# Optimization experiments

Hardware: AMD Instinct MI355X
Metric: run time of the kernel (lower is better)

The kernel has to match this reference:

```python
import jax, jax.numpy as jnp
import numpy as np

THRESHOLD_PERCENTILE = 0.8  # init arg
B, H, W, C, N = 4, 256, 256, 128, 32


def _label_components(mask):
    """8-connected components via iterative min-label propagation.
    Background pixels get sentinel label BIG (== scipy label 0)."""
    h, w = mask.shape
    big = h * w
    init = jnp.where(mask, jnp.arange(big, dtype=jnp.int32).reshape(h, w), jnp.int32(big))

    def propagate(lbl):
        p = jnp.pad(lbl, 1, constant_values=big)
        # min over the 3x3 (8-connected incl. self) neighborhood
        nb = jnp.min(jnp.stack([p[di:di + h, dj:dj + w]
                                for di in range(3) for dj in range(3)]), axis=0)
        return jnp.where(mask, nb, jnp.int32(big))

    def cond(state):
        return ~state[1]

    def body(state):
        lbl, _ = state
        new = propagate(lbl)
        return new, jnp.all(new == lbl)

    lbl, _ = jax.lax.while_loop(cond, body, (init, jnp.array(False)))
    return lbl, jnp.int32(big)


def _merged_pairs_one(feat, centers):
    """feat: [H,W,C] float; centers: [N,2] int32. Returns merged-pair count."""
    h, w, c = feat.shape
    gt = feat[centers[:, 0], centers[:, 1]]                    # [N,C]
    flat = feat.reshape(-1, c)                                 # [HW,C]
    # euclidean cdist via norms (torch.cdist p=2)
    d2 = (jnp.sum(flat * flat, axis=1)[:, None]
          + jnp.sum(gt * gt, axis=1)[None, :]
          - 2.0 * flat @ gt.T)                                 # [HW,N]
    dists = jnp.sqrt(jnp.maximum(d2, 0.0))
    contrast = dists.min(axis=1).reshape(h, w)                 # [H,W]
    thr = jnp.percentile(contrast, THRESHOLD_PERCENTILE * 100.0)
    mask = contrast >= thr
    lbl, big = _label_components(mask)
    ids = lbl[centers[:, 0], centers[:, 1]]                    # [N]
    valid = ids != big                                         # scipy label > 0
    eq = (ids[:, None] == ids[None, :]) & valid[:, None]
    n = centers.shape[0]
    triu = jnp.triu(jnp.ones((n, n), dtype=bool), 1)           # i < j pairs
    return jnp.sum(eq & triu)


def setup_inputs() -> dict:
    key = jax.random.key(0)
    k1, k2 = jax.random.split(key)
    features = jax.random.normal(k1, (B, H, W, C), dtype=jnp.float32)
    gt_centers = jax.random.randint(k2, (B, N, 2), 0, H, dtype=jnp.int64)
    return {"features": features, "gt_centers": gt_centers}


def reference(features, gt_centers):
    centers = gt_centers.astype(jnp.int32)
    merged = jax.vmap(_merged_pairs_one)(features, centers)    # [B]
    n = centers.shape[1]
    total_pairs = features.shape[0] * (n * (n - 1) // 2)
    merge_rate = merged.sum().astype(jnp.float32) / jnp.float32(total_pairs)
    return merge_rate
```

## Files before the change

kernel.cpp:

```cpp
#include <hip/hip_runtime.h>
#include <stdint.h>

#define BB 4
#define HH 256
#define WW 256
#define CC 128
#define NN 32
#define NPIX (HH*WW)
#define RANK 52428u
#define TOTAL_PAIRS 1984.0f
#define CAND_MAX 8192u

#define OFF_HIST 0
#define ZERO_BYTES (BB*1024*4)
#define OFF_THR  ZERO_BYTES
#define OFF_P    (OFF_THR + 64)
#define OFF_KEYS (OFF_P + BB*NPIX*4)

typedef __attribute__((ext_vector_type(8))) short short8;
typedef __attribute__((ext_vector_type(4))) float f32x4;

__device__ __forceinline__ void split3(float f, short &hi, short &mid, short &lo) {
    uint32_t u  = __float_as_uint(f);
    uint32_t hb = u & 0xffff0000u;
    hi = (short)(hb >> 16);
    float r1 = f - __uint_as_float(hb);
    uint32_t mb = __float_as_uint(r1) & 0xffff0000u;
    mid = (short)(mb >> 16);
    float r2 = r1 - __uint_as_float(mb);
    lo = (short)(__float_as_uint(r2) >> 16);
}

__device__ __forceinline__ uint32_t qbin_of(uint32_t keybits) {
    float f = __uint_as_float(keybits);
    return (uint32_t)fminf(f * 128.0f, 65535.0f);
}

__global__ __launch_bounds__(256) void k_d2mfma(const float* __restrict__ feat,
        const int* __restrict__ centers, uint32_t* __restrict__ keys,
        uint32_t* __restrict__ hist, int* __restrict__ Pg) {
    __shared__ short gB[12288];
    __shared__ float gpart[32][8];
    __shared__ float gnormL[32];
    __shared__ uint32_t lhist[1024];
    int b = blockIdx.y;
    int tid = threadIdx.x;

    Pg[(b << 16) + blockIdx.x*256 + tid] = 0;

    #pragma unroll
    for (int j = 0; j < 4; j++) lhist[tid + j*256] = 0u;

    {
        int n = tid & 31, j0 = tid >> 5;
        int cy = centers[(b*NN + n)*2 + 0];
        int cx = centers[(b*NN + n)*2 + 1];
        const float* gp = feat + ((size_t)(b << 16) + cy*WW + cx)*CC + j0*16;
        int tt = n >> 4, lane16 = n & 15, q_ = j0 >> 1, kkb = (j0 & 1)*2;
        float ss = 0.f;
        #pragma unroll
        for (int hh = 0; hh < 2; hh++) {
            short8 vhi, vmid, vlo;
            #pragma unroll
            for (int u = 0; u < 8; u++) {
                float f = gp[hh*8 + u];
                ss = fmaf(f, f, ss);
                short a, bm, c; split3(f, a, bm, c);
                vhi[u] = a; vmid[u] = bm; vlo[u] = c;
            }
            int lane = q_*16 + lane16;
            int off = (tt*4 + kkb + hh)*512 + lane*8;
            *(short8*)&gB[off]        = vhi;
            *(short8*)&gB[off + 4096] = vmid;
            *(short8*)&gB[off + 8192] = vlo;
        }
        gpart[n][j0] = ss;
    }
    __syncthreads();
    if (tid < 32) {
        float s = 0.f;
        #pragma unroll
        for (int j = 0; j < 8; j++) s += gpart[tid][j];
        gnormL[tid] = s;
    }
    __syncthreads();

    int wv = tid >> 6, L = tid & 63;
    int m = L & 15, q = L >> 4;
    float gn0 = gnormL[m];
    float gn1 = gnormL[16 + m];

    const float* fpl = feat + ((size_t)(b << 16) + blockIdx.x*256 + m)*CC + q*32;

    float4 pf[8];
    {
        const float* f0 = fpl + (size_t)(wv*4)*16*CC;
        #pragma unroll
        for (int j = 0; j < 8; j++) pf[j] = *(const float4*)(f0 + j*4);
    }

    #pragma unroll
    for (int it = 0; it < 4; it++) {
        int p0 = blockIdx.x*256 + (wv*4 + it)*16;

        float4 nf[8];
        if (it < 3) {
            const float* f1 = fpl + (size_t)(wv*4 + it + 1)*16*CC;
            #pragma unroll
            for (int j = 0; j < 8; j++) nf[j] = *(const float4*)(f1 + j*4);
        }

        f32x4 acc[2] = {{0.f,0.f,0.f,0.f},{0.f,0.f,0.f,0.f}};
        float fn = 0.f;

        #pragma unroll
        for (int kk = 0; kk < 4; kk++) {
            float4 fa = pf[kk*2];
            float4 fb = pf[kk*2 + 1];
            float fs[8] = {fa.x,fa.y,fa.z,fa.w,fb.x,fb.y,fb.z,fb.w};
            short8 ahi, amid, alo;
            #pragma unroll
            for (int j = 0; j < 8; j++) {
                float f = fs[j];
                fn = fmaf(f, f, fn);
                short hh, md, lw; split3(f, hh, md, lw);
                ahi[j] = hh; amid[j] = md; alo[j] = lw;
            }
            #pragma unroll
            for (int t = 0; t < 2; t++) {
                int off = (t*4 + kk)*512 + L*8;
                short8 bhi = *(const short8*)&gB[off];
                short8 bmd = *(const short8*)&gB[off + 4096];
                short8 blo = *(const short8*)&gB[off + 8192];
                acc[t] = __builtin_amdgcn_mfma_f32_16x16x32_bf16(ahi,  bhi, acc[t], 0,0,0);
                acc[t] = __builtin_amdgcn_mfma_f32_16x16x32_bf16(ahi,  bmd, acc[t], 0,0,0);
                acc[t] = __builtin_amdgcn_mfma_f32_16x16x32_bf16(amid, bhi, acc[t], 0,0,0);
                acc[t] = __builtin_amdgcn_mfma_f32_16x16x32_bf16(ahi,  blo, acc[t], 0,0,0);
                acc[t] = __builtin_amdgcn_mfma_f32_16x16x32_bf16(amid, bmd, acc[t], 0,0,0);
                acc[t] = __builtin_amdgcn_mfma_f32_16x16x32_bf16(alo,  bhi, acc[t], 0,0,0);
            }
        }

        fn += __shfl_xor(fn, 16);
        fn += __shfl_xor(fn, 32);

        float vmin[4];
        #pragma unroll
        for (int r = 0; r < 4; r++) {
            float fnr = __shfl(fn, q*4 + r);
            float d0 = fnr + gn0 - 2.f*acc[0][r];
            float d1 = fnr + gn1 - 2.f*acc[1][r];
            float v = fminf(d0, d1);
            v = fminf(v, __shfl_xor(v, 1));
            v = fminf(v, __shfl_xor(v, 2));
            v = fminf(v, __shfl_xor(v, 4));
            v = fminf(v, __shfl_xor(v, 8));
            vmin[r] = v;
        }
        if (m < 4) {
            float v = (m==0) ? vmin[0] : (m==1) ? vmin[1] : (m==2) ? vmin[2] : vmin[3];
            if (!(v > 0.f)) v = 0.f;
            uint32_t kb = __float_as_uint(v);
            keys[(size_t)(b << 16) + p0 + q*4 + m] = kb;
            atomicAdd(&lhist[qbin_of(kb) >> 6], 1u);
        }

        if (it < 3) {
            #pragma unroll
            for (int j = 0; j < 8; j++) pf[j] = nf[j];
        }
    }

    __syncthreads();
    #pragma unroll
    for (int j = 0; j < 4; j++) {
        int bin = tid + j*256;
        uint32_t hv = lhist[bin];
        if (hv) atomicAdd(&hist[(b << 10) + bin], hv);
    }
}

__global__ __launch_bounds__(1024) void k_selthr(const uint32_t* __restrict__ keys,
        const uint32_t* __restrict__ hist, uint32_t* __restrict__ thr_sm) {
    int b = blockIdx.x, t = threadIdx.x;
    __shared__ uint32_t wsum[16];
    __shared__ uint32_t sT1, sR1, sT, sR2, scnt, scnt2;
    __shared__ uint32_t fh[64];
    __shared__ uint32_t cand[CAND_MAX];
    __shared__ uint32_t cand2[2048];

    if (t < 64) fh[t] = 0;
    if (t == 0) { scnt = 0; scnt2 = 0; }

    int lane = t & 63, w = t >> 6;
    uint32_t s = hist[(b << 10) + t];
    uint32_t inc = s;
    #pragma unroll
    for (int off = 1; off < 64; off <<= 1) {
        uint32_t nb = __shfl_up((int)inc, off);
        if (lane >= off) inc += nb;
    }
    if (lane == 63) wsum[w] = inc;
    __syncthreads();
    if (t < 16) {
        uint32_t v = wsum[t];
        #pragma unroll
        for (int off = 1; off < 16; off <<= 1) {
            uint32_t nb = __shfl_up((int)v, off);
            if (t >= off) v += nb;
        }
        wsum[t] = v;
    }
    __syncthreads();
    uint32_t pre = ((w == 0) ? 0u : wsum[w-1]) + inc - s;
    if (pre <= RANK && RANK < pre + s) { sT1 = (uint32_t)t; sR1 = RANK - pre; }
    __syncthreads();
    uint32_t T1 = sT1, r1 = sR1;

    const uint4* kb = (const uint4*)(keys + ((size_t)b << 16));
    for (int i = t; i < NPIX/4; i += 1024) {
        uint4 k = kb[i];
        uint32_t q;
        #define PROC_KEY(X) { q = qbin_of(X); if ((q >> 6) == T1) { \
            atomicAdd(&fh[q & 63u], 1u); \
            uint32_t p = atomicAdd(&scnt, 1u); \
            if (p < CAND_MAX) cand[p] = (X); } }
        PROC_KEY(k.x) PROC_KEY(k.y) PROC_KEY(k.z) PROC_KEY(k.w)
        #undef PROC_KEY
    }
    __syncthreads();

    if (t < 64) {
        uint32_t s2 = fh[t];
        uint32_t inc2 = s2;
        #pragma unroll
        for (int off = 1; off < 64; off <<= 1) {
            uint32_t nb = __shfl_up((int)inc2, off);
            if (t >= off) inc2 += nb;
        }
        uint32_t pre2 = inc2 - s2;
        if (pre2 <= r1 && r1 < pre2 + s2) { sT = (T1 << 6) | (uint32_t)t; sR2 = r1 - pre2; }
    }
    __syncthreads();
    uint32_t T = sT, r2 = sR2;
    uint32_t K = scnt; if (K > CAND_MAX) K = CAND_MAX;

    for (uint32_t i = t; i < K; i += 1024) {
        uint32_t v = cand[i];
        if (qbin_of(v) == T) { uint32_t p = atomicAdd(&scnt2, 1u); if (p < 2048u) cand2[p] = v; }
    }
    __syncthreads();
    uint32_t K2 = scnt2; if (K2 > 2048u) K2 = 2048u;

    for (uint32_t i = t; i < K2; i += 1024) {
        uint32_t v = cand2[i];
        uint32_t less = 0, eq = 0;
        for (uint32_t j = 0; j < K2; j++) { uint32_t x = cand2[j]; less += (x < v); eq += (x == v); }
        if (less <= r2 && r2 < less + eq) thr_sm[b] = v;
    }
}

__device__ __forceinline__ int uf_find(int* P, int x) {
    while (true) {
        int v = P[x];
        if (v == 0) return x;
        int p = v - 1;
        int gv = P[p];
        if (gv == 0) return p;
        P[x] = gv;
        x = gv - 1;
    }
}
__device__ __forceinline__ void uf_unite(int* P, int a, int b) {
    while (true) {
        a = uf_find(P, a);
        b = uf_find(P, b);
        if (a == b) return;
        if (a > b) { int t = a; a = b; b = t; }
        int old = atomicCAS(&P[b], 0, a + 1);
        if (old == 0) return;
        b = old - 1;
    }
}

__global__ __launch_bounds__(256) void k_ccl(const uint32_t* __restrict__ keys,
        const uint32_t* __restrict__ thr_sm, int* __restrict__ Pg) {
    int bid = blockIdx.x;
    int b = bid >> 8, rr = bid & 255;
    int x = threadIdx.x;
    __shared__ int up_rs[256];
    __shared__ int swtmp[4];

    uint32_t thrv = thr_sm[b];
    int* P = Pg + (b << 16);
    int p = (rr << 8) + x;
    bool msk = keys[((size_t)b << 16) + p] >= thrv;
    int lane = x & 63, w = x >> 6;

    int v = msk ? -1 : x;
    #pragma unroll
    for (int off = 1; off < 64; off <<= 1) {
        int nb = __shfl_up(v, off);
        if (lane >= off) v = max(v, nb);
    }
    if (lane == 63) swtmp[w] = v;
    __syncthreads();
    int acc = v;
    for (int i = 0; i < w; i++) acc = max(acc, swtmp[i]);
    int rs = (rr << 8) + acc + 1;
    __syncthreads();

    if (rr > 0) {
        bool msku = keys[((size_t)b << 16) + p - WW] >= thrv;
        int vu = msku ? -1 : x;
        #pragma unroll
        for (int off = 1; off < 64; off <<= 1) {
            int nb = __shfl_up(vu, off);
            if (lane >= off) vu = max(vu, nb);
        }
        if (lane == 63) swtmp[w] = vu;
        __syncthreads();
        int accu = vu;
        for (int i = 0; i < w; i++) accu = max(accu, swtmp[i]);
        up_rs[x] = msku ? (((rr - 1) << 8) + accu + 1) : -1;
    }

    if (msk && rs != p) P[p] = rs + 1;
    __syncthreads();

    if (rr > 0 && msk) {
        bool ul = (x > 0)   && up_rs[x-1] >= 0;
        bool uu =              up_rs[x]   >= 0;
        bool ur = (x < 255) && up_rs[x+1] >= 0;
        if (ul)        uf_unite(P, rs, up_rs[x-1]);
        if (uu && !ul) uf_unite(P, rs, up_rs[x]);
        if (ur && !uu) uf_unite(P, rs, up_rs[x+1]);
    }
}

__global__ void k_pairs_fin(const int* __restrict__ centers,
        const uint32_t* __restrict__ keys, const uint32_t* __restrict__ thr_sm,
        const int* __restrict__ Pg, float* __restrict__ out) {
    __shared__ int ids[BB*NN];
    __shared__ int total;
    int t = threadIdx.x;
    if (t == 0) total = 0;
    __syncthreads();
    if (t < BB*NN) {
        int bb = t >> 5;
        int cy = centers[t*2 + 0];
        int cx = centers[t*2 + 1];
        int pp = cy*WW + cx;
        const int* Pb = Pg + (bb << 16);
        int id = -1;
        if (keys[((size_t)bb << 16) + pp] >= thr_sm[bb]) {
            int xx = pp;
            while (true) { int vv = Pb[xx]; if (vv == 0) break; xx = vv - 1; }
            id = xx;
        }
        ids[t] = id;
    }
    __syncthreads();
    int cnt = 0;
    if (t < BB*NN) {
        int bb = t >> 5, n = t & 31;
        int id = ids[t];
        if (id != -1) for (int j = n + 1; j < NN; j++) cnt += (ids[bb*NN + j] == id);
    }
    if (cnt) atomicAdd(&total, cnt);
    __syncthreads();
    if (t == 0) out[0] = (float)total / TOTAL_PAIRS;
}

extern "C" void kernel_launch(void* const* d_in, const int* in_sizes, int n_in,
                              void* d_out, int out_size, void* d_ws, size_t ws_size,
                              hipStream_t stream) {
    const float* feat  = (const float*)d_in[0];
    const int* centers = (const int*)d_in[1];
    float* out         = (float*)d_out;
    char* ws           = (char*)d_ws;

    uint32_t* hist = (uint32_t*)(ws + OFF_HIST);
    uint32_t* thr  = (uint32_t*)(ws + OFF_THR);
    int*      Pg   = (int*)(ws + OFF_P);
    uint32_t* keys = (uint32_t*)(ws + OFF_KEYS);

    hipMemsetAsync(ws, 0, ZERO_BYTES, stream);

    dim3 gridPix(NPIX/256, BB);
    k_d2mfma    <<<gridPix, 256, 0, stream>>>(feat, centers, keys, hist, Pg);
    k_selthr    <<<BB, 1024, 0, stream>>>(keys, hist, thr);
    k_ccl       <<<HH*BB, 256, 0, stream>>>(keys, thr, Pg);
    k_pairs_fin <<<1, 256, 0, stream>>>(centers, keys, thr, Pg, out);
}
```

Before: 224.6 us.

## Fuse threshold selection, CCL and pair counting into one per-image kernel

Merges the threshold-select, connected-component labeling and pair-count kernels into a single kernel with one 1024-thread block per image, and uses a global done-counter so the last block writes the result. This removes two kernel launches and the global threshold round-trip. The labeling loses the row-scan prepass and the 1024-block parallelism: only 4 blocks now do union-find over 65536 pixels each, neighbor by neighbor, so labeling may take much longer.

```diff
diff --git a/kernel.cpp b/kernel.cpp
--- a/kernel.cpp
+++ b/kernel.cpp
@@ -12,9 +12,9 @@
 #define CAND_MAX 8192u
 
 #define OFF_HIST 0
-#define ZERO_BYTES (BB*1024*4)
-#define OFF_THR  ZERO_BYTES
-#define OFF_P    (OFF_THR + 64)
+#define OFF_SYNC (BB*1024*4)
+#define ZERO_BYTES (OFF_SYNC + 256)
+#define OFF_P    ZERO_BYTES
 #define OFF_KEYS (OFF_P + BB*NPIX*4)
 
 typedef __attribute__((ext_vector_type(8))) short short8;
@@ -180,17 +180,44 @@
     }
 }
 
-__global__ __launch_bounds__(1024) void k_selthr(const uint32_t* __restrict__ keys,
-        const uint32_t* __restrict__ hist, uint32_t* __restrict__ thr_sm) {
+__device__ __forceinline__ int uf_find(int* P, int x) {
+    while (true) {
+        int v = P[x];
+        if (v == 0) return x;
+        int p = v - 1;
+        int gv = P[p];
+        if (gv == 0) return p;
+        P[x] = gv;
+        x = gv - 1;
+    }
+}
+__device__ __forceinline__ void uf_unite(int* P, int a, int b) {
+    while (true) {
+        a = uf_find(P, a);
+        b = uf_find(P, b);
+        if (a == b) return;
+        if (a > b) { int t = a; a = b; b = t; }
+        int old = atomicCAS(&P[b], 0, a + 1);
+        if (old == 0) return;
+        b = old - 1;
+    }
+}
+
+__global__ __launch_bounds__(1024) void k_tail(const uint32_t* __restrict__ keys,
+        const uint32_t* __restrict__ hist, const int* __restrict__ centers,
+        int* __restrict__ Pg, uint32_t* __restrict__ done, int* __restrict__ gcount,
+        float* __restrict__ out) {
     int b = blockIdx.x, t = threadIdx.x;
     __shared__ uint32_t wsum[16];
-    __shared__ uint32_t sT1, sR1, sT, sR2, scnt, scnt2;
+    __shared__ uint32_t sT1, sR1, sT, sR2, scnt, scnt2, sThr;
     __shared__ uint32_t fh[64];
     __shared__ uint32_t cand[CAND_MAX];
     __shared__ uint32_t cand2[2048];
+    __shared__ int ids[NN];
+    __shared__ int blkcnt;
 
     if (t < 64) fh[t] = 0;
-    if (t == 0) { scnt = 0; scnt2 = 0; }
+    if (t == 0) { scnt = 0; scnt2 = 0; blkcnt = 0; }
 
     int lane = t & 63, w = t >> 6;
     uint32_t s = hist[(b << 10) + t];
@@ -256,120 +283,56 @@
         uint32_t v = cand2[i];
         uint32_t less = 0, eq = 0;
         for (uint32_t j = 0; j < K2; j++) { uint32_t x = cand2[j]; less += (x < v); eq += (x == v); }
-        if (less <= r2 && r2 < less + eq) thr_sm[b] = v;
-    }
-}
-
-__device__ __forceinline__ int uf_find(int* P, int x) {
-    while (true) {
-        int v = P[x];
-        if (v == 0) return x;
-        int p = v - 1;
-        int gv = P[p];
-        if (gv == 0) return p;
-        P[x] = gv;
-        x = gv - 1;
-    }
-}
-__device__ __forceinline__ void uf_unite(int* P, int a, int b) {
-    while (true) {
-        a = uf_find(P, a);
-        b = uf_find(P, b);
-        if (a == b) return;
-        if (a > b) { int t = a; a = b; b = t; }
-        int old = atomicCAS(&P[b], 0, a + 1);
-        if (old == 0) return;
-        b = old - 1;
-    }
-}
-
-__global__ __launch_bounds__(256) void k_ccl(const uint32_t* __restrict__ keys,
-        const uint32_t* __restrict__ thr_sm, int* __restrict__ Pg) {
-    int bid = blockIdx.x;
-    int b = bid >> 8, rr = bid & 255;
-    int x = threadIdx.x;
-    __shared__ int up_rs[256];
-    __shared__ int swtmp[4];
-
-    uint32_t thrv = thr_sm[b];
+        if (less <= r2 && r2 < less + eq) sThr = v;
+    }
+    __syncthreads();
+    uint32_t thrv = sThr;
+
+    const uint32_t* kf = keys + ((size_t)b << 16);
     int* P = Pg + (b << 16);
-    int p = (rr << 8) + x;
-    bool msk = keys[((size_t)b << 16) + p] >= thrv;
-    int lane = x & 63, w = x >> 6;
-
-    int v = msk ? -1 : x;
-    #pragma unroll
-    for (int off = 1; off < 64; off <<= 1) {
-        int nb = __shfl_up(v, off);
-        if (lane >= off) v = max(v, nb);
-    }
-    if (lane == 63) swtmp[w] = v;
-    __syncthreads();
-    int acc = v;
-    for (int i = 0; i < w; i++) acc = max(acc, swtmp[i]);
-    int rs = (rr << 8) + acc + 1;
-    __syncthreads();
-
-    if (rr > 0) {
-        bool msku = keys[((size_t)b << 16) + p - WW] >= thrv;
-        int vu = msku ? -1 : x;
-        #pragma unroll
-        for (int off = 1; off < 64; off <<= 1) {
-            int nb = __shfl_up(vu, off);
-            if (lane >= off) vu = max(vu, nb);
-        }
-        if (lane == 63) swtmp[w] = vu;
-        __syncthreads();
-        int accu = vu;
-        for (int i = 0; i < w; i++) accu = max(accu, swtmp[i]);
-        up_rs[x] = msku ? (((rr - 1) << 8) + accu + 1) : -1;
-    }
-
-    if (msk && rs != p) P[p] = rs + 1;
-    __syncthreads();
-
-    if (rr > 0 && msk) {
-        bool ul = (x > 0)   && up_rs[x-1] >= 0;
-        bool uu =              up_rs[x]   >= 0;
-        bool ur = (x < 255) && up_rs[x+1] >= 0;
-        if (ul)        uf_unite(P, rs, up_rs[x-1]);
-        if (uu && !ul) uf_unite(P, rs, up_rs[x]);
-        if (ur && !uu) uf_unite(P, rs, up_rs[x+1]);
-    }
-}
-
-__global__ void k_pairs_fin(const int* __restrict__ centers,
-        const uint32_t* __restrict__ keys, const uint32_t* __restrict__ thr_sm,
-        const int* __restrict__ Pg, float* __restrict__ out) {
-    __shared__ int ids[BB*NN];
-    __shared__ int total;
-    int t = threadIdx.x;
-    if (t == 0) total = 0;
-    __syncthreads();
-    if (t < BB*NN) {
-        int bb = t >> 5;
-        int cy = centers[t*2 + 0];
-        int cx = centers[t*2 + 1];
+    for (int i = t; i < NPIX; i += 1024) {
+        if (kf[i] < thrv) continue;
+        int x = i & 255, y = i >> 8;
+        if (x > 0 && kf[i-1] >= thrv) uf_unite(P, i, i-1);
+        if (y > 0) {
+            if (kf[i-WW] >= thrv)              uf_unite(P, i, i-WW);
+            if (x > 0   && kf[i-WW-1] >= thrv) uf_unite(P, i, i-WW-1);
+            if (x < 255 && kf[i-WW+1] >= thrv) uf_unite(P, i, i-WW+1);
+        }
+    }
+    __syncthreads();
+
+    if (t < NN) {
+        int cy = centers[(b*NN + t)*2 + 0];
+        int cx = centers[(b*NN + t)*2 + 1];
         int pp = cy*WW + cx;
-        const int* Pb = Pg + (bb << 16);
         int id = -1;
-        if (keys[((size_t)bb << 16) + pp] >= thr_sm[bb]) {
+        if (kf[pp] >= thrv) {
             int xx = pp;
-            while (true) { int vv = Pb[xx]; if (vv == 0) break; xx = vv - 1; }
+            while (true) { int vv = P[xx]; if (vv == 0) break; xx = vv - 1; }
             id = xx;
         }
         ids[t] = id;
     }
     __syncthreads();
     int cnt = 0;
-    if (t < BB*NN) {
-        int bb = t >> 5, n = t & 31;
+    if (t < NN) {
         int id = ids[t];
-        if (id != -1) for (int j = n + 1; j < NN; j++) cnt += (ids[bb*NN + j] == id);
-    }
-    if (cnt) atomicAdd(&total, cnt);
-    __syncthreads();
-    if (t == 0) out[0] = (float)total / TOTAL_PAIRS;
+        if (id != -1) for (int j = t + 1; j < NN; j++) cnt += (ids[j] == id);
+    }
+    if (cnt) atomicAdd(&blkcnt, cnt);
+    __syncthreads();
+
+    if (t == 0) {
+        atomicAdd(gcount, blkcnt);
+        __threadfence();
+        uint32_t d = atomicAdd(done, 1u);
+        if (d == 3u) {
+            __threadfence();
+            int total = atomicAdd(gcount, 0);
+            out[0] = (float)total / TOTAL_PAIRS;
+        }
+    }
 }
 
 extern "C" void kernel_launch(void* const* d_in, const int* in_sizes, int n_in,
@@ -380,16 +343,15 @@
     float* out         = (float*)d_out;
     char* ws           = (char*)d_ws;
 
-    uint32_t* hist = (uint32_t*)(ws + OFF_HIST);
-    uint32_t* thr  = (uint32_t*)(ws + OFF_THR);
-    int*      Pg   = (int*)(ws + OFF_P);
-    uint32_t* keys = (uint32_t*)(ws + OFF_KEYS);
+    uint32_t* hist   = (uint32_t*)(ws + OFF_HIST);
+    uint32_t* done   = (uint32_t*)(ws + OFF_SYNC);
+    int*      gcount = (int*)(ws + OFF_SYNC + 4);
+    int*      Pg     = (int*)(ws + OFF_P);
+    uint32_t* keys   = (uint32_t*)(ws + OFF_KEYS);
 
     hipMemsetAsync(ws, 0, ZERO_BYTES, stream);
 
     dim3 gridPix(NPIX/256, BB);
-    k_d2mfma    <<<gridPix, 256, 0, stream>>>(feat, centers, keys, hist, Pg);
-    k_selthr    <<<BB, 1024, 0, stream>>>(keys, hist, thr);
-    k_ccl       <<<HH*BB, 256, 0, stream>>>(keys, thr, Pg);
-    k_pairs_fin <<<1, 256, 0, stream>>>(centers, keys, thr, Pg, out);
-}
+    k_d2mfma <<<gridPix, 256, 0, stream>>>(feat, centers, keys, hist, Pg);
+    k_tail   <<<BB, 1024, 0, stream>>>(keys, hist, centers, Pg, done, gcount, out);
+}
```

Result: slower. 678.7 us (+202.2%).

## Move coarse histogram from distance kernel into threshold-selection kernel

Applied to the files above, without the earlier changes.

The coarse 1024-bin histogram of contrast keys used to be built in the distance kernel with shared-memory atomics and then flushed to global memory, which needed a memset launch beforehand. It is now built inside the threshold-selection kernel by rereading the keys of each image. This removes the memset launch, the LDS histogram and the global atomics from the wide distance kernel. The cost is an extra pass over 64K keys per image, done by only 4 blocks in a serial part of the pipeline.

```diff
diff --git a/kernel.cpp b/kernel.cpp
--- a/kernel.cpp
+++ b/kernel.cpp
@@ -11,10 +11,8 @@
 #define TOTAL_PAIRS 1984.0f
 #define CAND_MAX 8192u
 
-#define OFF_HIST 0
-#define ZERO_BYTES (BB*1024*4)
-#define OFF_THR  ZERO_BYTES
-#define OFF_P    (OFF_THR + 64)
+#define OFF_THR  0
+#define OFF_P    64
 #define OFF_KEYS (OFF_P + BB*NPIX*4)
 
 typedef __attribute__((ext_vector_type(8))) short short8;
@@ -38,18 +36,14 @@
 
 __global__ __launch_bounds__(256) void k_d2mfma(const float* __restrict__ feat,
         const int* __restrict__ centers, uint32_t* __restrict__ keys,
-        uint32_t* __restrict__ hist, int* __restrict__ Pg) {
+        int* __restrict__ Pg) {
     __shared__ short gB[12288];
     __shared__ float gpart[32][8];
     __shared__ float gnormL[32];
-    __shared__ uint32_t lhist[1024];
     int b = blockIdx.y;
     int tid = threadIdx.x;
 
     Pg[(b << 16) + blockIdx.x*256 + tid] = 0;
-
-    #pragma unroll
-    for (int j = 0; j < 4; j++) lhist[tid + j*256] = 0u;
 
     {
         int n = tid & 31, j0 = tid >> 5;
@@ -160,9 +154,7 @@
         if (m < 4) {
             float v = (m==0) ? vmin[0] : (m==1) ? vmin[1] : (m==2) ? vmin[2] : vmin[3];
             if (!(v > 0.f)) v = 0.f;
-            uint32_t kb = __float_as_uint(v);
-            keys[(size_t)(b << 16) + p0 + q*4 + m] = kb;
-            atomicAdd(&lhist[qbin_of(kb) >> 6], 1u);
+            keys[(size_t)(b << 16) + p0 + q*4 + m] = __float_as_uint(v);
         }
 
         if (it < 3) {
@@ -170,30 +162,35 @@
             for (int j = 0; j < 8; j++) pf[j] = nf[j];
         }
     }
-
-    __syncthreads();
-    #pragma unroll
-    for (int j = 0; j < 4; j++) {
-        int bin = tid + j*256;
-        uint32_t hv = lhist[bin];
-        if (hv) atomicAdd(&hist[(b << 10) + bin], hv);
-    }
 }
 
 __global__ __launch_bounds__(1024) void k_selthr(const uint32_t* __restrict__ keys,
-        const uint32_t* __restrict__ hist, uint32_t* __restrict__ thr_sm) {
+        uint32_t* __restrict__ thr_sm) {
     int b = blockIdx.x, t = threadIdx.x;
+    __shared__ uint32_t h1[1024];
     __shared__ uint32_t wsum[16];
     __shared__ uint32_t sT1, sR1, sT, sR2, scnt, scnt2;
     __shared__ uint32_t fh[64];
     __shared__ uint32_t cand[CAND_MAX];
     __shared__ uint32_t cand2[2048];
 
+    h1[t] = 0;
     if (t < 64) fh[t] = 0;
     if (t == 0) { scnt = 0; scnt2 = 0; }
+    __syncthreads();
+
+    const uint4* kb = (const uint4*)(keys + ((size_t)b << 16));
+    for (int i = t; i < NPIX/4; i += 1024) {
+        uint4 k = kb[i];
+        atomicAdd(&h1[qbin_of(k.x) >> 6], 1u);
+        atomicAdd(&h1[qbin_of(k.y) >> 6], 1u);
+        atomicAdd(&h1[qbin_of(k.z) >> 6], 1u);
+        atomicAdd(&h1[qbin_of(k.w) >> 6], 1u);
+    }
+    __syncthreads();
 
     int lane = t & 63, w = t >> 6;
-    uint32_t s = hist[(b << 10) + t];
+    uint32_t s = h1[t];
     uint32_t inc = s;
     #pragma unroll
     for (int off = 1; off < 64; off <<= 1) {
@@ -217,7 +214,6 @@
     __syncthreads();
     uint32_t T1 = sT1, r1 = sR1;
 
-    const uint4* kb = (const uint4*)(keys + ((size_t)b << 16));
     for (int i = t; i < NPIX/4; i += 1024) {
         uint4 k = kb[i];
         uint32_t q;
@@ -380,16 +376,13 @@
     float* out         = (float*)d_out;
     char* ws           = (char*)d_ws;
 
-    uint32_t* hist = (uint32_t*)(ws + OFF_HIST);
     uint32_t* thr  = (uint32_t*)(ws + OFF_THR);
     int*      Pg   = (int*)(ws + OFF_P);
     uint32_t* keys = (uint32_t*)(ws + OFF_KEYS);
 
-    hipMemsetAsync(ws, 0, ZERO_BYTES, stream);
-
     dim3 gridPix(NPIX/256, BB);
-    k_d2mfma    <<<gridPix, 256, 0, stream>>>(feat, centers, keys, hist, Pg);
-    k_selthr    <<<BB, 1024, 0, stream>>>(keys, hist, thr);
+    k_d2mfma    <<<gridPix, 256, 0, stream>>>(feat, centers, keys, Pg);
+    k_selthr    <<<BB, 1024, 0, stream>>>(keys, thr);
     k_ccl       <<<HH*BB, 256, 0, stream>>>(keys, thr, Pg);
     k_pairs_fin <<<1, 256, 0, stream>>>(centers, keys, thr, Pg, out);
 }
```

Result: no change. 225.6 us (+0.5%).
